# Performance work log

Measured on AMD Instinct MI355X. Metric: run time of the kernel, lower is better.

Reference implementation:

```python
import jax, jax.numpy as jnp
import numpy as np

N_QUBITS = 4
N_LAYERS = 1
B, D_IN, D_OUT = 65536, 1024, 1024

def _cnot_perm(c, t):
    idx = np.arange(16)
    cb = (idx >> (3 - c)) & 1
    return idx ^ (cb << (3 - t))  # involutive permutation

CNOT_PERMS = [_cnot_perm(i, (i + 1) % N_QUBITS) for i in range(N_QUBITS)]
_idx = np.arange(16)
Z_SIGNS = np.stack([1.0 - 2.0 * ((_idx >> (3 - i)) & 1) for i in range(N_QUBITS)]).astype(np.float32)  # [4,16]
H_GATE = (np.array([[1, 1], [1, -1]]) / np.sqrt(2.0)).astype(np.complex64)

def _apply_1q(psi, U, wire):
    # psi: [B,2,2,2,2]; U: [2,2] (shared across batch)
    psi = jnp.moveaxis(psi, wire + 1, -1)
    psi = jnp.einsum('b...j,ij->b...i', psi, U)
    return jnp.moveaxis(psi, -1, wire + 1)

def _apply_1q_batched(psi, U, wire):
    # U: [B,2,2] (per-sample gate)
    psi = jnp.moveaxis(psi, wire + 1, -1)
    psi = jnp.einsum('b...j,bij->b...i', psi, U)
    return jnp.moveaxis(psi, -1, wire + 1)

def _ry_batched(th):
    c = jnp.cos(th / 2).astype(jnp.complex64)
    s = jnp.sin(th / 2).astype(jnp.complex64)
    return jnp.stack([jnp.stack([c, -s], -1), jnp.stack([s, c], -1)], -2)  # [B,2,2]

def _rz_batched(th):
    e = jnp.exp(-0.5j * th)  # complex64
    z = jnp.zeros_like(e)
    return jnp.stack([jnp.stack([e, z], -1), jnp.stack([z, jnp.conj(e)], -1)], -2)

def _rot(phi, th, om):
    # PennyLane Rot(phi,theta,omega) = RZ(omega) RY(theta) RZ(phi)
    c = jnp.cos(th / 2)
    s = jnp.sin(th / 2)
    return jnp.stack([
        jnp.stack([jnp.exp(-0.5j * (phi + om)) * c, -jnp.exp(0.5j * (phi - om)) * s]),
        jnp.stack([jnp.exp(-0.5j * (phi - om)) * s, jnp.exp(0.5j * (phi + om)) * c])])

def _circuit(angles, weights):
    # angles: [B,4] float; weights: [n_layers,4,3]; returns <Z_i> per wire: [B,4]
    b = angles.shape[0]
    psi = jnp.zeros((b, 16), jnp.complex64).at[:, 0].set(1.0).reshape(b, 2, 2, 2, 2)
    H = jnp.asarray(H_GATE)
    for i in range(N_QUBITS):
        psi = _apply_1q(psi, H, i)
        f = angles[:, i]
        psi = _apply_1q_batched(psi, _ry_batched(jnp.arctan(f)), i)
        psi = _apply_1q_batched(psi, _rz_batched(jnp.arctan(f ** 2)), i)
    for l in range(N_LAYERS):
        for i in range(N_QUBITS):
            psi = psi.reshape(b, 16)[:, CNOT_PERMS[i]].reshape(b, 2, 2, 2, 2)
        for i in range(N_QUBITS):
            U = _rot(weights[l, i, 0], weights[l, i, 1], weights[l, i, 2])
            psi = _apply_1q(psi, U, i)
    psi_f = psi.reshape(b, 16)
    probs = psi_f.real ** 2 + psi_f.imag ** 2  # [B,16] float32
    return probs @ jnp.asarray(Z_SIGNS).T  # [B,4]

def setup_inputs() -> dict:
    key = jax.random.key(0)
    k = jax.random.split(key, 6)
    scale_pre = 1.0 / np.sqrt(D_IN)
    scale_post = 1.0 / np.sqrt(N_QUBITS)
    return {
        'x': jax.random.normal(k[0], (B, D_IN), jnp.float32),
        'pre_w': jax.random.normal(k[1], (N_QUBITS, D_IN), jnp.float32) * scale_pre,
        'pre_b': jax.random.normal(k[2], (N_QUBITS,), jnp.float32) * scale_pre,
        'q_weights': jax.random.uniform(k[3], (N_LAYERS, N_QUBITS, 3), jnp.float32) * (2.0 * np.pi),
        'post_w': jax.random.normal(k[4], (D_OUT, N_QUBITS), jnp.float32) * scale_post,
        'post_b': jax.random.normal(k[5], (D_OUT,), jnp.float32) * scale_post,
    }

def reference(x, pre_w, pre_b, q_weights, post_w, post_b):
    h = jnp.tanh(x @ pre_w.T + pre_b) * np.pi  # [B,4]
    z = _circuit(h, q_weights).astype(jnp.float32)  # [B,4]
    return z @ post_w.T + post_b  # [B,1024]
```

## Files before the change

### kernel.cpp

```cpp
#include <hip/hip_runtime.h>
#include <math.h>

#define D_IN_K  1024
#define D_OUT_K 1024

static constexpr float PI_F = 3.14159265358979323846f;

__device__ __forceinline__ float dot4(float4 a, float4 b, float acc) {
    return fmaf(a.x, b.x, fmaf(a.y, b.y, fmaf(a.z, b.z, fmaf(a.w, b.w, acc))));
}

__global__ __launch_bounds__(256) void pre_kernel(
    const float* __restrict__ x, const float* __restrict__ pw,
    const float* __restrict__ pb, float* __restrict__ h, int B)
{
    const int wave = threadIdx.x >> 6;
    const int lane = threadIdx.x & 63;
    const int row0 = blockIdx.x * 16 + wave * 4;
    if (row0 >= B) return;

    const float4* w0 = reinterpret_cast<const float4*>(pw);
    const float4* w1 = reinterpret_cast<const float4*>(pw + D_IN_K);
    const float4* w2 = reinterpret_cast<const float4*>(pw + 2 * D_IN_K);
    const float4* w3 = reinterpret_cast<const float4*>(pw + 3 * D_IN_K);
    const float4* x0 = reinterpret_cast<const float4*>(x + (size_t)(row0 + 0) * D_IN_K);
    const float4* x1 = reinterpret_cast<const float4*>(x + (size_t)(row0 + 1) * D_IN_K);
    const float4* x2 = reinterpret_cast<const float4*>(x + (size_t)(row0 + 2) * D_IN_K);
    const float4* x3 = reinterpret_cast<const float4*>(x + (size_t)(row0 + 3) * D_IN_K);

    float acc[4][4];
#pragma unroll
    for (int r = 0; r < 4; ++r)
#pragma unroll
        for (int q = 0; q < 4; ++q) acc[r][q] = 0.f;

#pragma unroll
    for (int k = 0; k < 4; ++k) {
        const int idx = lane + (k << 6);
        float4 a = w0[idx], b = w1[idx], c = w2[idx], d = w3[idx];
        float4 xv;
        xv = x0[idx];
        acc[0][0] = dot4(xv, a, acc[0][0]); acc[0][1] = dot4(xv, b, acc[0][1]);
        acc[0][2] = dot4(xv, c, acc[0][2]); acc[0][3] = dot4(xv, d, acc[0][3]);
        xv = x1[idx];
        acc[1][0] = dot4(xv, a, acc[1][0]); acc[1][1] = dot4(xv, b, acc[1][1]);
        acc[1][2] = dot4(xv, c, acc[1][2]); acc[1][3] = dot4(xv, d, acc[1][3]);
        xv = x2[idx];
        acc[2][0] = dot4(xv, a, acc[2][0]); acc[2][1] = dot4(xv, b, acc[2][1]);
        acc[2][2] = dot4(xv, c, acc[2][2]); acc[2][3] = dot4(xv, d, acc[2][3]);
        xv = x3[idx];
        acc[3][0] = dot4(xv, a, acc[3][0]); acc[3][1] = dot4(xv, b, acc[3][1]);
        acc[3][2] = dot4(xv, c, acc[3][2]); acc[3][3] = dot4(xv, d, acc[3][3]);
    }

#pragma unroll
    for (int off = 1; off < 64; off <<= 1) {
#pragma unroll
        for (int r = 0; r < 4; ++r)
#pragma unroll
            for (int q = 0; q < 4; ++q)
                acc[r][q] += __shfl_xor(acc[r][q], off, 64);
    }

    float v = acc[0][0];
#pragma unroll
    for (int r = 0; r < 4; ++r)
#pragma unroll
        for (int q = 0; q < 4; ++q)
            if (lane == r * 4 + q) v = acc[r][q];

    if (lane < 16) {
        float s = tanhf(v + pb[lane & 3]) * PI_F;
        h[(size_t)row0 * 4 + lane] = s;
    }
}

template <int MASK>
__device__ __forceinline__ void apply1q(
    float* pr, float* pim,
    float u00r, float u00i, float u01r, float u01i,
    float u10r, float u10i, float u11r, float u11i)
{
#pragma unroll
    for (int j = 0; j < 16; ++j) {
        if (j & MASK) continue;
        const int k = j | MASK;
        float a0r = pr[j], a0i = pim[j], a1r = pr[k], a1i = pim[k];
        pr[j]  = u00r * a0r - u00i * a0i + u01r * a1r - u01i * a1i;
        pim[j] = u00r * a0i + u00i * a0r + u01r * a1i + u01i * a1r;
        pr[k]  = u10r * a0r - u10i * a0i + u11r * a1r - u11i * a1i;
        pim[k] = u10r * a0i + u10i * a0r + u11r * a1i + u11i * a1r;
    }
}

template <int CMASK, int TMASK>
__device__ __forceinline__ void cnot(float* pr, float* pim)
{
#pragma unroll
    for (int j = 0; j < 16; ++j) {
        if ((j & CMASK) && !(j & TMASK)) {
            const int k = j | TMASK;
            float t;
            t = pr[j];  pr[j]  = pr[k];  pr[k]  = t;
            t = pim[j]; pim[j] = pim[k]; pim[k] = t;
        }
    }
}

template <int MASK>
__device__ __forceinline__ void encode_qubit(float* pr, float* pim, float f)
{
    const float r = 0.70710678118654752440f;
    apply1q<MASK>(pr, pim, r, 0.f, r, 0.f, r, 0.f, -r, 0.f);
    float th = atanf(f) * 0.5f;
    float s, c;
    sincosf(th, &s, &c);
    apply1q<MASK>(pr, pim, c, 0.f, -s, 0.f, s, 0.f, c, 0.f);
    float al = atanf(f * f) * 0.5f;
    float sa, ca;
    sincosf(al, &sa, &ca);
    apply1q<MASK>(pr, pim, ca, -sa, 0.f, 0.f, 0.f, 0.f, ca, sa);
}

template <int MASK>
__device__ __forceinline__ void rot_qubit(float* pr, float* pim,
                                          float phi, float th, float om)
{
    float st, ct, sp, cp, sm, cm;
    sincosf(0.5f * th, &st, &ct);
    sincosf(0.5f * (phi + om), &sp, &cp);
    sincosf(0.5f * (phi - om), &sm, &cm);
    apply1q<MASK>(pr, pim,
                  ct * cp, -ct * sp,
                  -st * cm, -st * sm,
                  st * cm, -st * sm,
                  ct * cp, ct * sp);
}

__global__ __launch_bounds__(256) void circuit_kernel(
    const float* __restrict__ h, const float* __restrict__ qw,
    float* __restrict__ z, int B)
{
    int b = blockIdx.x * 256 + threadIdx.x;
    if (b >= B) return;

    float4 hv = reinterpret_cast<const float4*>(h)[b];

    float pr[16], pim[16];
#pragma unroll
    for (int j = 0; j < 16; ++j) { pr[j] = 0.f; pim[j] = 0.f; }
    pr[0] = 1.f;

    encode_qubit<8>(pr, pim, hv.x);
    encode_qubit<4>(pr, pim, hv.y);
    encode_qubit<2>(pr, pim, hv.z);
    encode_qubit<1>(pr, pim, hv.w);

    cnot<8, 4>(pr, pim);
    cnot<4, 2>(pr, pim);
    cnot<2, 1>(pr, pim);
    cnot<1, 8>(pr, pim);

    rot_qubit<8>(pr, pim, qw[0], qw[1], qw[2]);
    rot_qubit<4>(pr, pim, qw[3], qw[4], qw[5]);
    rot_qubit<2>(pr, pim, qw[6], qw[7], qw[8]);
    rot_qubit<1>(pr, pim, qw[9], qw[10], qw[11]);

    float z0 = 0.f, z1 = 0.f, z2 = 0.f, z3 = 0.f;
#pragma unroll
    for (int j = 0; j < 16; ++j) {
        float p = pr[j] * pr[j] + pim[j] * pim[j];
        z0 += (j & 8) ? -p : p;
        z1 += (j & 4) ? -p : p;
        z2 += (j & 2) ? -p : p;
        z3 += (j & 1) ? -p : p;
    }
    float4 zv;
    zv.x = z0; zv.y = z1; zv.z = z2; zv.w = z3;
    reinterpret_cast<float4*>(z)[b] = zv;
}

__global__ __launch_bounds__(256) void post_kernel(
    const float* __restrict__ z, const float* __restrict__ pw,
    const float* __restrict__ pb, float* __restrict__ out, int B)
{
    const int t = threadIdx.x;
    const int row0 = blockIdx.x * 16;
    if (row0 >= B) return;

    const float4* pwv = reinterpret_cast<const float4*>(pw);
    float4 w[4];
    float bias[4];
#pragma unroll
    for (int j = 0; j < 4; ++j) {
        w[j]    = pwv[t + 256 * j];
        bias[j] = pb[t + 256 * j];
    }

    const float4* zv = reinterpret_cast<const float4*>(z);
#pragma unroll
    for (int r = 0; r < 16; ++r) {
        float4 zr = zv[row0 + r];
        float* orow = out + (size_t)(row0 + r) * D_OUT_K;
#pragma unroll
        for (int j = 0; j < 4; ++j) {
            float o = fmaf(zr.x, w[j].x,
                      fmaf(zr.y, w[j].y,
                      fmaf(zr.z, w[j].z,
                      fmaf(zr.w, w[j].w, bias[j]))));
            orow[t + 256 * j] = o;
        }
    }
}

extern "C" void kernel_launch(void* const* d_in, const int* in_sizes, int n_in,
                              void* d_out, int out_size, void* d_ws, size_t ws_size,
                              hipStream_t stream)
{
    const float* x      = (const float*)d_in[0];
    const float* pre_w  = (const float*)d_in[1];
    const float* pre_b  = (const float*)d_in[2];
    const float* qw     = (const float*)d_in[3];
    const float* post_w = (const float*)d_in[4];
    const float* post_b = (const float*)d_in[5];
    float* out = (float*)d_out;

    const int B = in_sizes[0] / D_IN_K;

    float* h = (float*)d_ws;
    float* z = h + (size_t)B * 4;

    pre_kernel<<<(B + 15) / 16, 256, 0, stream>>>(x, pre_w, pre_b, h, B);
    circuit_kernel<<<(B + 255) / 256, 256, 0, stream>>>(h, qw, z, B);
    post_kernel<<<(B + 15) / 16, 256, 0, stream>>>(z, post_w, post_b, out, B);
}
```

Baseline: 473.3 us.

## Fuse pre-projection, quantum circuit and post-projection into one kernel

```diff
diff --git a/kernel.cpp b/kernel.cpp
--- a/kernel.cpp
+++ b/kernel.cpp
@@ -10,23 +10,100 @@
     return fmaf(a.x, b.x, fmaf(a.y, b.y, fmaf(a.z, b.z, fmaf(a.w, b.w, acc))));
 }
 
-__global__ __launch_bounds__(256) void pre_kernel(
+template <int MASK>
+__device__ __forceinline__ void apply1q(
+    float* pr, float* pim,
+    float u00r, float u00i, float u01r, float u01i,
+    float u10r, float u10i, float u11r, float u11i)
+{
+#pragma unroll
+    for (int j = 0; j < 16; ++j) {
+        if (j & MASK) continue;
+        const int k = j | MASK;
+        float a0r = pr[j], a0i = pim[j], a1r = pr[k], a1i = pim[k];
+        pr[j]  = u00r * a0r - u00i * a0i + u01r * a1r - u01i * a1i;
+        pim[j] = u00r * a0i + u00i * a0r + u01r * a1i + u01i * a1r;
+        pr[k]  = u10r * a0r - u10i * a0i + u11r * a1r - u11i * a1i;
+        pim[k] = u10r * a0i + u10i * a0r + u11r * a1i + u11i * a1r;
+    }
+}
+
+template <int CMASK, int TMASK>
+__device__ __forceinline__ void cnot(float* pr, float* pim)
+{
+#pragma unroll
+    for (int j = 0; j < 16; ++j) {
+        if ((j & CMASK) && !(j & TMASK)) {
+            const int k = j | TMASK;
+            float t;
+            t = pr[j];  pr[j]  = pr[k];  pr[k]  = t;
+            t = pim[j]; pim[j] = pim[k]; pim[k] = t;
+        }
+    }
+}
+
+template <int MASK>
+__device__ __forceinline__ void encode_qubit(float* pr, float* pim, float f)
+{
+    const float r = 0.70710678118654752440f;
+    apply1q<MASK>(pr, pim, r, 0.f, r, 0.f, r, 0.f, -r, 0.f);
+    float th = atanf(f) * 0.5f;
+    float s, c;
+    sincosf(th, &s, &c);
+    apply1q<MASK>(pr, pim, c, 0.f, -s, 0.f, s, 0.f, c, 0.f);
+    float al = atanf(f * f) * 0.5f;
+    float sa, ca;
+    sincosf(al, &sa, &ca);
+    apply1q<MASK>(pr, pim, ca, -sa, 0.f, 0.f, 0.f, 0.f, ca, sa);
+}
+
+template <int MASK>
+__device__ __forceinline__ void rot_qubit(float* pr, float* pim,
+                                          float phi, float th, float om)
+{
+    float st, ct, sp, cp, sm, cm;
+    sincosf(0.5f * th, &st, &ct);
+    sincosf(0.5f * (phi + om), &sp, &cp);
+    sincosf(0.5f * (phi - om), &sm, &cm);
+    apply1q<MASK>(pr, pim,
+                  ct * cp, -ct * sp,
+                  -st * cm, -st * sm,
+                  st * cm, -st * sm,
+                  ct * cp, ct * sp);
+}
+
+__global__ __launch_bounds__(256) void fused_kernel(
     const float* __restrict__ x, const float* __restrict__ pw,
-    const float* __restrict__ pb, float* __restrict__ h, int B)
-{
-    const int wave = threadIdx.x >> 6;
-    const int lane = threadIdx.x & 63;
-    const int row0 = blockIdx.x * 16 + wave * 4;
+    const float* __restrict__ pb, const float* __restrict__ qw,
+    const float* __restrict__ postw, const float* __restrict__ postb,
+    float* __restrict__ out, int B)
+{
+    const int t    = threadIdx.x;
+    const int wave = t >> 6;
+    const int lane = t & 63;
+    const int row0  = blockIdx.x * 16;
+    const int wrow0 = row0 + wave * 4;
     if (row0 >= B) return;
+
+    __shared__ float4 zlds[16];
+
+    const float4* pwv4 = reinterpret_cast<const float4*>(postw);
+    float4 w[4];
+    float bias[4];
+#pragma unroll
+    for (int j = 0; j < 4; ++j) {
+        w[j]    = pwv4[t + 256 * j];
+        bias[j] = postb[t + 256 * j];
+    }
 
     const float4* w0 = reinterpret_cast<const float4*>(pw);
     const float4* w1 = reinterpret_cast<const float4*>(pw + D_IN_K);
     const float4* w2 = reinterpret_cast<const float4*>(pw + 2 * D_IN_K);
     const float4* w3 = reinterpret_cast<const float4*>(pw + 3 * D_IN_K);
-    const float4* x0 = reinterpret_cast<const float4*>(x + (size_t)(row0 + 0) * D_IN_K);
-    const float4* x1 = reinterpret_cast<const float4*>(x + (size_t)(row0 + 1) * D_IN_K);
-    const float4* x2 = reinterpret_cast<const float4*>(x + (size_t)(row0 + 2) * D_IN_K);
-    const float4* x3 = reinterpret_cast<const float4*>(x + (size_t)(row0 + 3) * D_IN_K);
+    const float4* x0 = reinterpret_cast<const float4*>(x + (size_t)(wrow0 + 0) * D_IN_K);
+    const float4* x1 = reinterpret_cast<const float4*>(x + (size_t)(wrow0 + 1) * D_IN_K);
+    const float4* x2 = reinterpret_cast<const float4*>(x + (size_t)(wrow0 + 2) * D_IN_K);
+    const float4* x3 = reinterpret_cast<const float4*>(x + (size_t)(wrow0 + 3) * D_IN_K);
 
     float acc[4][4];
 #pragma unroll
@@ -62,145 +139,50 @@
                 acc[r][q] += __shfl_xor(acc[r][q], off, 64);
     }
 
-    float v = acc[0][0];
-#pragma unroll
-    for (int r = 0; r < 4; ++r)
+    if (lane < 4) {
+        const int r = lane;
+        float hq[4];
 #pragma unroll
         for (int q = 0; q < 4; ++q)
-            if (lane == r * 4 + q) v = acc[r][q];
-
-    if (lane < 16) {
-        float s = tanhf(v + pb[lane & 3]) * PI_F;
-        h[(size_t)row0 * 4 + lane] = s;
-    }
-}
-
-template <int MASK>
-__device__ __forceinline__ void apply1q(
-    float* pr, float* pim,
-    float u00r, float u00i, float u01r, float u01i,
-    float u10r, float u10i, float u11r, float u11i)
-{
-#pragma unroll
-    for (int j = 0; j < 16; ++j) {
-        if (j & MASK) continue;
-        const int k = j | MASK;
-        float a0r = pr[j], a0i = pim[j], a1r = pr[k], a1i = pim[k];
-        pr[j]  = u00r * a0r - u00i * a0i + u01r * a1r - u01i * a1i;
-        pim[j] = u00r * a0i + u00i * a0r + u01r * a1i + u01i * a1r;
-        pr[k]  = u10r * a0r - u10i * a0i + u11r * a1r - u11i * a1i;
-        pim[k] = u10r * a0i + u10i * a0r + u11r * a1i + u11i * a1r;
-    }
-}
-
-template <int CMASK, int TMASK>
-__device__ __forceinline__ void cnot(float* pr, float* pim)
-{
-#pragma unroll
-    for (int j = 0; j < 16; ++j) {
-        if ((j & CMASK) && !(j & TMASK)) {
-            const int k = j | TMASK;
-            float t;
-            t = pr[j];  pr[j]  = pr[k];  pr[k]  = t;
-            t = pim[j]; pim[j] = pim[k]; pim[k] = t;
+            hq[q] = tanhf(acc[r][q] + pb[q]) * PI_F;
+
+        float pr[16], pim[16];
+#pragma unroll
+        for (int j = 0; j < 16; ++j) { pr[j] = 0.f; pim[j] = 0.f; }
+        pr[0] = 1.f;
+
+        encode_qubit<8>(pr, pim, hq[0]);
+        encode_qubit<4>(pr, pim, hq[1]);
+        encode_qubit<2>(pr, pim, hq[2]);
+        encode_qubit<1>(pr, pim, hq[3]);
+
+        cnot<8, 4>(pr, pim);
+        cnot<4, 2>(pr, pim);
+        cnot<2, 1>(pr, pim);
+        cnot<1, 8>(pr, pim);
+
+        rot_qubit<8>(pr, pim, qw[0], qw[1], qw[2]);
+        rot_qubit<4>(pr, pim, qw[3], qw[4], qw[5]);
+        rot_qubit<2>(pr, pim, qw[6], qw[7], qw[8]);
+        rot_qubit<1>(pr, pim, qw[9], qw[10], qw[11]);
+
+        float z0 = 0.f, z1 = 0.f, z2 = 0.f, z3 = 0.f;
+#pragma unroll
+        for (int j = 0; j < 16; ++j) {
+            float p = pr[j] * pr[j] + pim[j] * pim[j];
+            z0 += (j & 8) ? -p : p;
+            z1 += (j & 4) ? -p : p;
+            z2 += (j & 2) ? -p : p;
+            z3 += (j & 1) ? -p : p;
         }
-    }
-}
-
-template <int MASK>
-__device__ __forceinline__ void encode_qubit(float* pr, float* pim, float f)
-{
-    const float r = 0.70710678118654752440f;
-    apply1q<MASK>(pr, pim, r, 0.f, r, 0.f, r, 0.f, -r, 0.f);
-    float th = atanf(f) * 0.5f;
-    float s, c;
-    sincosf(th, &s, &c);
-    apply1q<MASK>(pr, pim, c, 0.f, -s, 0.f, s, 0.f, c, 0.f);
-    float al = atanf(f * f) * 0.5f;
-    float sa, ca;
-    sincosf(al, &sa, &ca);
-    apply1q<MASK>(pr, pim, ca, -sa, 0.f, 0.f, 0.f, 0.f, ca, sa);
-}
-
-template <int MASK>
-__device__ __forceinline__ void rot_qubit(float* pr, float* pim,
-                                          float phi, float th, float om)
-{
-    float st, ct, sp, cp, sm, cm;
-    sincosf(0.5f * th, &st, &ct);
-    sincosf(0.5f * (phi + om), &sp, &cp);
-    sincosf(0.5f * (phi - om), &sm, &cm);
-    apply1q<MASK>(pr, pim,
-                  ct * cp, -ct * sp,
-                  -st * cm, -st * sm,
-                  st * cm, -st * sm,
-                  ct * cp, ct * sp);
-}
-
-__global__ __launch_bounds__(256) void circuit_kernel(
-    const float* __restrict__ h, const float* __restrict__ qw,
-    float* __restrict__ z, int B)
-{
-    int b = blockIdx.x * 256 + threadIdx.x;
-    if (b >= B) return;
-
-    float4 hv = reinterpret_cast<const float4*>(h)[b];
-
-    float pr[16], pim[16];
-#pragma unroll
-    for (int j = 0; j < 16; ++j) { pr[j] = 0.f; pim[j] = 0.f; }
-    pr[0] = 1.f;
-
-    encode_qubit<8>(pr, pim, hv.x);
-    encode_qubit<4>(pr, pim, hv.y);
-    encode_qubit<2>(pr, pim, hv.z);
-    encode_qubit<1>(pr, pim, hv.w);
-
-    cnot<8, 4>(pr, pim);
-    cnot<4, 2>(pr, pim);
-    cnot<2, 1>(pr, pim);
-    cnot<1, 8>(pr, pim);
-
-    rot_qubit<8>(pr, pim, qw[0], qw[1], qw[2]);
-    rot_qubit<4>(pr, pim, qw[3], qw[4], qw[5]);
-    rot_qubit<2>(pr, pim, qw[6], qw[7], qw[8]);
-    rot_qubit<1>(pr, pim, qw[9], qw[10], qw[11]);
-
-    float z0 = 0.f, z1 = 0.f, z2 = 0.f, z3 = 0.f;
-#pragma unroll
-    for (int j = 0; j < 16; ++j) {
-        float p = pr[j] * pr[j] + pim[j] * pim[j];
-        z0 += (j & 8) ? -p : p;
-        z1 += (j & 4) ? -p : p;
-        z2 += (j & 2) ? -p : p;
-        z3 += (j & 1) ? -p : p;
-    }
-    float4 zv;
-    zv.x = z0; zv.y = z1; zv.z = z2; zv.w = z3;
-    reinterpret_cast<float4*>(z)[b] = zv;
-}
-
-__global__ __launch_bounds__(256) void post_kernel(
-    const float* __restrict__ z, const float* __restrict__ pw,
-    const float* __restrict__ pb, float* __restrict__ out, int B)
-{
-    const int t = threadIdx.x;
-    const int row0 = blockIdx.x * 16;
-    if (row0 >= B) return;
-
-    const float4* pwv = reinterpret_cast<const float4*>(pw);
-    float4 w[4];
-    float bias[4];
-#pragma unroll
-    for (int j = 0; j < 4; ++j) {
-        w[j]    = pwv[t + 256 * j];
-        bias[j] = pb[t + 256 * j];
-    }
-
-    const float4* zv = reinterpret_cast<const float4*>(z);
+        float4 zv; zv.x = z0; zv.y = z1; zv.z = z2; zv.w = z3;
+        zlds[wave * 4 + r] = zv;
+    }
+    __syncthreads();
+
 #pragma unroll
     for (int r = 0; r < 16; ++r) {
-        float4 zr = zv[row0 + r];
+        float4 zr = zlds[r];
         float* orow = out + (size_t)(row0 + r) * D_OUT_K;
 #pragma unroll
         for (int j = 0; j < 4; ++j) {
@@ -227,10 +209,8 @@
 
     const int B = in_sizes[0] / D_IN_K;
 
-    float* h = (float*)d_ws;
-    float* z = h + (size_t)B * 4;
-
-    pre_kernel<<<(B + 15) / 16, 256, 0, stream>>>(x, pre_w, pre_b, h, B);
-    circuit_kernel<<<(B + 255) / 256, 256, 0, stream>>>(h, qw, z, B);
-    post_kernel<<<(B + 15) / 16, 256, 0, stream>>>(z, post_w, post_b, out, B);
-}
+    (void)d_ws; (void)ws_size;
+
+    fused_kernel<<<(B + 15) / 16, 256, 0, stream>>>(
+        x, pre_w, pre_b, qw, post_w, post_b, out, B);
+}
```

New measurement: 445.5 us. 5.9% less time.
